# Optimization experiments

Measured on AMD Instinct MI355X. Metric: run time of the kernel, lower is better.

## Reference

```python
import jax, jax.numpy as jnp
import numpy as np

B, T, PHYS = 256, 64, 3        # batch of initial conditions, time steps, physical dim
LAT, NN, NHID = 8, 128, 3      # latent dim, hidden width, num hidden layers
WIN, PRED = 32, 64             # Hankel window, num_pred_steps


def _mlp(x, w_in, b_in, w_h, b_h, w_out, b_out):
    # Dense stack: relu hidden layers, linear output (ae_output_activation='linear')
    h = jax.nn.relu(x @ w_in + b_in)
    for i in range(w_h.shape[0]):
        h = jax.nn.relu(h @ w_h[i] + b_h[i])
    return h @ w_out + b_out


def _hankel_dmd(y):
    # y: [B, L, T] latent trajectories (already transposed as in call())
    Bsz, L, Tn = y.shape
    R = Tn - (WIN - 1)                                   # num_rows_hankel
    # Vectorized Hankel build (replaces nested TensorArray loops):
    idx = jnp.arange(R)[:, None] + jnp.arange(WIN)[None, :]
    H = y[:, :, idx].reshape(Bsz, L * R, WIN)
    Ym, Yp = H[:, :, :-1], H[:, :, 1:]
    # Exact DMD operator A = Yp V Sig^-1 U^H (full M x M, as in the TF code)
    U, sig, Vh = jnp.linalg.svd(Ym, full_matrices=False)
    V = jnp.swapaxes(Vh, -1, -2)
    A = Yp @ (V / sig[:, None, :]) @ jnp.swapaxes(U, -1, -2)     # [B, M, M]
    A = jax.lax.stop_gradient(A)   # no-op in fwd; eig has no JAX grad rule
    evals, evecs = jnp.linalg.eig(A)                             # complex64: [B,M], [B,M,M]
    Phi = jnp.linalg.solve(evecs, Ym.astype(evecs.dtype))
    y0 = Phi[:, :, 0]                                            # [B, M]
    evecs_s = evecs[:, ::R, :]                                   # stride = R -> [B, L, M]
    # Vectorized replacement of the sequential recon loop: evals^k for k=0..P-1
    powers = evals[:, None, :] ** jnp.arange(PRED)[None, :, None]  # [B, P, M]
    modes = powers * y0[:, None, :]                                # [B, P, M]
    recon = jnp.real(jnp.einsum('blm,bpm->bpl', evecs_s, modes))   # [B, P, L]
    return recon


def setup_inputs() -> dict:
    ks = jax.random.split(jax.random.key(0), 8)

    def w(k, fi, fo):
        return jax.random.normal(k, (fi, fo), jnp.float32) / np.sqrt(fi)

    def wh(k, f):
        return jax.random.normal(k, (NHID, f, f), jnp.float32) / np.sqrt(f)

    return {
        'x': jax.random.normal(ks[0], (B, T, PHYS), jnp.float32),
        'enc_w_in': w(ks[1], PHYS, NN), 'enc_b_in': jnp.zeros((NN,), jnp.float32),
        'enc_w_h': wh(ks[2], NN), 'enc_b_h': jnp.zeros((NHID, NN), jnp.float32),
        'enc_w_out': w(ks[3], NN, LAT), 'enc_b_out': jnp.zeros((LAT,), jnp.float32),
        'dec_w_in': w(ks[4], LAT, NN), 'dec_b_in': jnp.zeros((NN,), jnp.float32),
        'dec_w_h': wh(ks[5], NN), 'dec_b_h': jnp.zeros((NHID, NN), jnp.float32),
        'dec_w_out': w(ks[6], NN, PHYS), 'dec_b_out': jnp.zeros((PHYS,), jnp.float32),
    }


def reference(x, enc_w_in, enc_b_in, enc_w_h, enc_b_h, enc_w_out, enc_b_out,
              dec_w_in, dec_b_in, dec_w_h, dec_b_h, dec_w_out, dec_b_out):
    y = _mlp(x, enc_w_in, enc_b_in, enc_w_h, enc_b_h, enc_w_out, enc_b_out)        # [B, T, LAT]
    x_ae = _mlp(y, dec_w_in, dec_b_in, dec_w_h, dec_b_h, dec_w_out, dec_b_out)     # [B, T, PHYS]
    y_adv = _hankel_dmd(jnp.swapaxes(y, 1, 2))                                     # [B, PRED, LAT]
    x_adv = _mlp(y_adv, dec_w_in, dec_b_in, dec_w_h, dec_b_h, dec_w_out, dec_b_out)  # [B, PRED, PHYS]
    return (y, x_ae, x_adv, y_adv)
```

## Files before the change

kernel.cpp:

```cpp
#include <hip/hip_runtime.h>
#include <math.h>

namespace {
constexpr int kB = 256;
constexpr int kT = 64;
constexpr int kPhys = 3;
constexpr int kLat = 8;
constexpr int kNN = 128;
constexpr int kWin = 32;
constexpr int kPred = 64;
constexpr int kHRow = 132;
constexpr int kDecRows = 96;
constexpr int kThreads = 1024;
constexpr int kWUnit = 8 * 4 * 64 * 8;
}

typedef short bf16x8 __attribute__((ext_vector_type(8)));
typedef float f32x4 __attribute__((ext_vector_type(4)));

__device__ __forceinline__ double rdlane_f64(double x, int l) {
  const long long v = __double_as_longlong(x);
  const int lo = __builtin_amdgcn_readlane((int)(unsigned int)(v & 0xffffffffll), l);
  const int hi = __builtin_amdgcn_readlane((int)(v >> 32), l);
  const long long r = (((long long)hi) << 32) | (unsigned long long)(unsigned int)lo;
  return __longlong_as_double(r);
}

__device__ __forceinline__ unsigned rneb(float f) {
  const unsigned u = __float_as_uint(f);
  return (u + 0x7fffu + ((u >> 16) & 1u)) >> 16;
}
__device__ __forceinline__ void split3(float a, short& s1, short& s2, short& s3) {
  const unsigned b1 = rneb(a);
  const float f1 = __uint_as_float(b1 << 16);
  const float r1 = a - f1;
  const unsigned b2 = rneb(r1);
  const float f2 = __uint_as_float(b2 << 16);
  s1 = (short)b1; s2 = (short)b2; s3 = (short)rneb(r1 - f2);
}
__device__ __forceinline__ void split2(float a, short& s1, short& s2) {
  const unsigned b1 = rneb(a);
  const float f1 = __uint_as_float(b1 << 16);
  s1 = (short)b1; s2 = (short)rneb(a - f1);
}

__global__ __launch_bounds__(256) void split_weights_kernel(
    const float* __restrict__ ewh, const float* __restrict__ dwh,
    short* __restrict__ wfrag)
{
  const int gid = blockIdx.x * 256 + threadIdx.x;
  const int l = gid & 63;
  const int q = (gid >> 6) & 3;
  const int n = (gid >> 8) & 7;
  const int layer = gid >> 11;
  const bool enc = layer < 3;
  const float* __restrict__ W = enc ? (ewh + (size_t)layer * kNN * kNN)
                                    : (dwh + (size_t)(layer - 3) * kNN * kNN);
  const int colg = 16 * n + (l & 15);
  const int krow = 8 * (l >> 4);
  bf16x8 p1, p2, p3;
#pragma unroll
  for (int e = 0; e < 8; ++e) {
    const float wv = W[(32 * q + krow + e) * kNN + colg];
    short s1, s2, s3; split3(wv, s1, s2, s3);
    p1[e] = s1; p2[e] = s2; p3[e] = s3;
  }
  const int off = ((n * 4 + q) * 64 + l) * 8;
  if (enc) {
    const size_t base = (size_t)(layer * 3) * kWUnit;
    *(bf16x8*)&wfrag[base + off] = p1;
    *(bf16x8*)&wfrag[base + kWUnit + off] = p2;
    *(bf16x8*)&wfrag[base + 2 * kWUnit + off] = p3;
  } else {
    const size_t base = (size_t)(9 + (layer - 3) * 2) * kWUnit;
    *(bf16x8*)&wfrag[base + off] = p1;
    *(bf16x8*)&wfrag[base + kWUnit + off] = p2;
  }
}

template<int MT, int SPLITS>
__device__ __forceinline__ void pack_frag(const float* __restrict__ hb,
                                          short* __restrict__ frag, int tid)
{
  constexpr int PLANE = MT * 4 * 64 * 8;
  for (int idx = tid; idx < MT * 256; idx += kThreads) {
    const int m = idx >> 8, q = (idx >> 6) & 3, l = idx & 63;
    const int row = 16 * m + (l & 15), col = 32 * q + 8 * (l >> 4);
    const float4 f0 = *(const float4*)&hb[row * kHRow + col];
    const float4 f1 = *(const float4*)&hb[row * kHRow + col + 4];
    const float f[8] = {f0.x, f0.y, f0.z, f0.w, f1.x, f1.y, f1.z, f1.w};
    bf16x8 p1, p2, p3;
#pragma unroll
    for (int e = 0; e < 8; ++e) {
      if constexpr (SPLITS == 3) {
        short s1, s2, s3; split3(f[e], s1, s2, s3);
        p1[e] = s1; p2[e] = s2; p3[e] = s3;
      } else {
        short s1, s2; split2(f[e], s1, s2);
        p1[e] = s1; p2[e] = s2;
      }
    }
    const int o = ((m * 4 + q) * 64 + l) * 8;
    *(bf16x8*)&frag[o] = p1;
    *(bf16x8*)&frag[PLANE + o] = p2;
    if constexpr (SPLITS == 3) *(bf16x8*)&frag[2 * PLANE + o] = p3;
  }
}

template<int MPW, int SPLITS>
__device__ __forceinline__ void mfma_layer(
    const short* __restrict__ Bfrag, const float* __restrict__ bias,
    const short* __restrict__ frag, float* __restrict__ hb, int tid)
{
  constexpr int MT = 2 * MPW;
  constexpr int PLANE = MT * 4 * 64 * 8;
  const int w = tid >> 6, l = tid & 63;
  const int n = w & 7, m0 = (w >> 3) * MPW;
  const int colg = 16 * n + (l & 15);
  bf16x8 B1[4], B2[4], B3[4];
#pragma unroll
  for (int q = 0; q < 4; ++q) {
    const int boff = ((n * 4 + q) * 64 + l) * 8;
    B1[q] = *(const bf16x8*)&Bfrag[boff];
    B2[q] = *(const bf16x8*)&Bfrag[kWUnit + boff];
    if constexpr (SPLITS == 3) B3[q] = *(const bf16x8*)&Bfrag[2 * kWUnit + boff];
  }
  const float bj = bias[colg];
  f32x4 acc[MPW];
#pragma unroll
  for (int mi = 0; mi < MPW; ++mi) acc[mi] = {bj, bj, bj, bj};
#pragma unroll
  for (int q = 0; q < 4; ++q) {
#pragma unroll
    for (int mi = 0; mi < MPW; ++mi) {
      const int o = (((m0 + mi) * 4 + q) * 64 + l) * 8;
      const bf16x8 a1 = *(const bf16x8*)&frag[o];
      const bf16x8 a2 = *(const bf16x8*)&frag[PLANE + o];
      acc[mi] = __builtin_amdgcn_mfma_f32_16x16x32_bf16(a1, B1[q], acc[mi], 0, 0, 0);
      acc[mi] = __builtin_amdgcn_mfma_f32_16x16x32_bf16(a1, B2[q], acc[mi], 0, 0, 0);
      acc[mi] = __builtin_amdgcn_mfma_f32_16x16x32_bf16(a2, B1[q], acc[mi], 0, 0, 0);
      if constexpr (SPLITS == 3) {
        const bf16x8 a3 = *(const bf16x8*)&frag[2 * PLANE + o];
        acc[mi] = __builtin_amdgcn_mfma_f32_16x16x32_bf16(a1, B3[q], acc[mi], 0, 0, 0);
        acc[mi] = __builtin_amdgcn_mfma_f32_16x16x32_bf16(a2, B2[q], acc[mi], 0, 0, 0);
        acc[mi] = __builtin_amdgcn_mfma_f32_16x16x32_bf16(a3, B1[q], acc[mi], 0, 0, 0);
      }
    }
  }
  const int rbase = (l >> 4) * 4;
#pragma unroll
  for (int mi = 0; mi < MPW; ++mi)
#pragma unroll
    for (int r = 0; r < 4; ++r)
      hb[(16 * (m0 + mi) + rbase + r) * kHRow + colg] = fmaxf(acc[mi][r], 0.f);
}

__global__ __launch_bounds__(kThreads, 4) void fused_kernel(
    const float* __restrict__ x,
    const float* __restrict__ ewin, const float* __restrict__ ebin,
    const float* __restrict__ ebh,
    const float* __restrict__ ewout,const float* __restrict__ ebout,
    const float* __restrict__ dwin, const float* __restrict__ dbin,
    const float* __restrict__ dbh,
    const float* __restrict__ dwout,const float* __restrict__ dbout,
    const short* __restrict__ wfrag,
    float* __restrict__ y_g, float* __restrict__ xae_g,
    float* __restrict__ xadv_g, float* __restrict__ yadv_g)
{
  __shared__ float hb[kDecRows * kHRow];
  __shared__ __align__(16) char fragbuf[49152];
  __shared__ float ybuf[kT][kLat + 1];
  __shared__ float yadv2[kWin][kLat + 1];
  __shared__ float inb[kT][4];

  short* frag = (short*)fragbuf;
  double* dmd = (double*)fragbuf;
  double* yd   = dmd;
  double* P    = dmd + 520;
  double* Corr = dmd + 2664;
  double* KTm  = dmd + 3720;
  double* Dv   = dmd + 4743;

  const int tid = threadIdx.x;
  const int b = blockIdx.x;

  const float* __restrict__ xg = x + (size_t)b * kT * kPhys;
  for (int i = tid; i < kT * kPhys; i += kThreads) inb[i / 3][i % 3] = xg[i];
  __syncthreads();

  {
    const int j = tid & 127, rg = tid >> 7;
    const float w0 = ewin[j], w1 = ewin[kNN + j], w2 = ewin[2 * kNN + j];
    const float bj = ebin[j];
#pragma unroll
    for (int rr = 0; rr < 8; ++rr) {
      const int r = rg * 8 + rr;
      hb[r * kHRow + j] = fmaxf(bj + inb[r][0] * w0 + inb[r][1] * w1 + inb[r][2] * w2, 0.f);
    }
  }
  __syncthreads();

#pragma unroll
  for (int L = 0; L < 3; ++L) {
    pack_frag<4, 3>(hb, frag, tid);
    __syncthreads();
    mfma_layer<2, 3>(wfrag + (size_t)(L * 3) * kWUnit, ebh + L * kNN, frag, hb, tid);
    __syncthreads();
  }

  if (tid < 512) {
    const int r = tid >> 3, o = tid & 7;
    float a = ebout[o];
    for (int k4 = 0; k4 < kNN; k4 += 4) {
      const float4 hv = *(const float4*)&hb[r * kHRow + k4];
      a += hv.x * ewout[(k4 + 0) * kLat + o] + hv.y * ewout[(k4 + 1) * kLat + o]
         + hv.z * ewout[(k4 + 2) * kLat + o] + hv.w * ewout[(k4 + 3) * kLat + o];
    }
    ybuf[r][o] = a;
    y_g[(size_t)b * kT * kLat + tid] = a;
    yd[o * 65 + r] = (double)a;
  }
  __syncthreads();

  {
    for (int idx = tid; idx < 32 * 64; idx += kThreads) {
      const int d = idx >> 6, t = idx & 63;
      if (t + d < kT) {
        double s = 0.0;
#pragma unroll
        for (int l = 0; l < kLat; ++l) s += yd[l * 65 + t] * yd[l * 65 + t + d];
        P[d * 67 + t] = s;
      }
    }
    __syncthreads();

    {
      const int a = tid >> 5, c = tid & 31;
      const int d = (c >= a) ? (c - a) : (a - c);
      const int base = (c >= a) ? a : c;
      double s0 = 0.0, s1 = 0.0;
#pragma unroll
      for (int r = 0; r < 32; r += 2) { s0 += P[d * 67 + base + r]; s1 += P[d * 67 + base + r + 1]; }
      Corr[a * 33 + c] = s0 + s1 + P[d * 67 + base + 32];
    }
    __syncthreads();

    if (tid < 64) {
      const int lane = tid;
      const int colidx = (lane <= 30) ? lane : (lane <= 61 ? lane - 30 : 1);
      double m[31];
#pragma unroll
      for (int i = 0; i < 31; ++i) m[i] = Corr[i * 33 + colidx];
#pragma unroll
      for (int k = 0; k < 31; ++k) {
        const double piv = rdlane_f64(m[k], k);
        const double pinv = 1.0 / piv;
        m[k] *= pinv;
#pragma unroll
        for (int i = 0; i < 31; ++i) {
          if (i == k) continue;
          const double bci = rdlane_f64(m[i], k);
          m[i] = fma(-bci, m[k], m[i]);
        }
      }
      if (lane >= 31 && lane < 62) {
        const int c = lane - 31;
#pragma unroll
        for (int i = 0; i < 31; ++i) KTm[i * 33 + c] = m[i];
      }
      const int ri = (lane < 31) ? lane : 0;
      double Kr[31];
#pragma unroll
      for (int j = 0; j < 31; ++j) Kr[j] = KTm[ri * 33 + j];

      double dv = Kr[30];
      if (lane < 31) Dv[0 * 33 + lane] = dv;
      for (int k = 0; k < 31; ++k) {
        double a0 = 0.0, a1 = 0.0, a2 = 0.0, a3 = 0.0;
#pragma unroll
        for (int j = 0; j < 31; ++j) {
          const double dj = rdlane_f64(dv, j);
          if ((j & 3) == 0) a0 = fma(Kr[j], dj, a0);
          else if ((j & 3) == 1) a1 = fma(Kr[j], dj, a1);
          else if ((j & 3) == 2) a2 = fma(Kr[j], dj, a2);
          else a3 = fma(Kr[j], dj, a3);
        }
        dv = (a0 + a1) + (a2 + a3);
        if (lane < 31) Dv[(k + 1) * 33 + lane] = dv;
      }
    }
    __syncthreads();

    float* __restrict__ ob = yadv_g + (size_t)b * kPred * kLat;
    if (tid < 256) {
      ob[tid] = ybuf[tid >> 3][tid & 7];
    } else if (tid < 512) {
      const int q = tid - 256;
      const int k = q >> 3, l = q & 7;
      double a0 = 0.0, a1 = 0.0, a2 = 0.0, a3 = 0.0;
#pragma unroll
      for (int j = 0; j < 31; ++j) {
        const double t = yd[l * 65 + j + 1];
        if ((j & 3) == 0) a0 = fma(t, Dv[k * 33 + j], a0);
        else if ((j & 3) == 1) a1 = fma(t, Dv[k * 33 + j], a1);
        else if ((j & 3) == 2) a2 = fma(t, Dv[k * 33 + j], a2);
        else a3 = fma(t, Dv[k * 33 + j], a3);
      }
      const float v = (float)((a0 + a1) + (a2 + a3));
      ob[256 + q] = v;
      yadv2[k][l] = v;
    }
    __syncthreads();
  }

  {
    const int j = tid & 127, rg = tid >> 7;
    float wr[kLat];
#pragma unroll
    for (int k = 0; k < kLat; ++k) wr[k] = dwin[k * kNN + j];
    const float bj = dbin[j];
#pragma unroll
    for (int rr = 0; rr < 12; ++rr) {
      const int r = rg * 12 + rr;
      const float* __restrict__ src = (r < kT) ? &ybuf[r][0] : &yadv2[r - kT][0];
      float a = bj;
#pragma unroll
      for (int k = 0; k < kLat; ++k) a += src[k] * wr[k];
      hb[r * kHRow + j] = fmaxf(a, 0.f);
    }
  }
  __syncthreads();

#pragma unroll
  for (int L = 0; L < 3; ++L) {
    pack_frag<6, 2>(hb, frag, tid);
    __syncthreads();
    mfma_layer<3, 2>(wfrag + (size_t)(9 + L * 2) * kWUnit, dbh + L * kNN, frag, hb, tid);
    __syncthreads();
  }

  for (int idx = tid; idx < kDecRows * kPhys; idx += kThreads) {
    const int r = idx / 3, o = idx - r * 3;
    float a = dbout[o];
    for (int k4 = 0; k4 < kNN; k4 += 4) {
      const float4 hv = *(const float4*)&hb[r * kHRow + k4];
      a += hv.x * dwout[(k4 + 0) * kPhys + o] + hv.y * dwout[(k4 + 1) * kPhys + o]
         + hv.z * dwout[(k4 + 2) * kPhys + o] + hv.w * dwout[(k4 + 3) * kPhys + o];
    }
    if (r < kT) {
      xae_g[(size_t)b * kT * kPhys + idx] = a;
      if (r < kWin) xadv_g[(size_t)b * kT * kPhys + idx] = a;
    } else {
      const int rr = r - kT + kWin;
      xadv_g[(size_t)b * kT * kPhys + rr * kPhys + o] = a;
    }
  }
}

extern "C" void kernel_launch(void* const* d_in, const int* in_sizes, int n_in,
                              void* d_out, int out_size, void* d_ws, size_t ws_size,
                              hipStream_t stream)
{
  const float* x         = (const float*)d_in[0];
  const float* enc_w_in  = (const float*)d_in[1];
  const float* enc_b_in  = (const float*)d_in[2];
  const float* enc_w_h   = (const float*)d_in[3];
  const float* enc_b_h   = (const float*)d_in[4];
  const float* enc_w_out = (const float*)d_in[5];
  const float* enc_b_out = (const float*)d_in[6];
  const float* dec_w_in  = (const float*)d_in[7];
  const float* dec_b_in  = (const float*)d_in[8];
  const float* dec_w_h   = (const float*)d_in[9];
  const float* dec_b_h   = (const float*)d_in[10];
  const float* dec_w_out = (const float*)d_in[11];
  const float* dec_b_out = (const float*)d_in[12];

  float* out   = (float*)d_out;
  float* y     = out;
  float* x_ae  = out + (size_t)kB * kT * kLat;
  float* x_adv = x_ae + (size_t)kB * kT * kPhys;
  float* y_adv = x_adv + (size_t)kB * kT * kPhys;

  short* wfrag = (short*)d_ws;

  split_weights_kernel<<<48, 256, 0, stream>>>(enc_w_h, dec_w_h, wfrag);
  fused_kernel<<<kB, kThreads, 0, stream>>>(
      x, enc_w_in, enc_b_in, enc_b_h, enc_w_out, enc_b_out,
      dec_w_in, dec_b_in, dec_b_h, dec_w_out, dec_b_out,
      wfrag, y, x_ae, x_adv, y_adv);
}
```

Before: 57.19 us.

## Halve block to 512 threads and process MLP rows in two chunks

The block size drops from 1024 to 512 threads. The encoder and decoder MLP stacks now run on two row chunks (32 rows for the encoder, 48 for the decoder) instead of all rows at once. The hidden buffer and the fragment buffer share one union shared-memory region, which cuts LDS per block so more blocks can be resident per CU. The cost is roughly twice as many barriers and serial layer passes per block, and the weight fragments are reloaded for each chunk.

New measurement: 123.0 us. 115% more time.

```diff
diff --git a/kernel.cpp b/kernel.cpp
--- a/kernel.cpp
+++ b/kernel.cpp
@@ -10,8 +10,7 @@
 constexpr int kWin = 32;
 constexpr int kPred = 64;
 constexpr int kHRow = 132;
-constexpr int kDecRows = 96;
-constexpr int kThreads = 1024;
+constexpr int kThreads = 512;
 constexpr int kWUnit = 8 * 4 * 64 * 8;
 }
 
@@ -107,15 +106,13 @@
   }
 }
 
-template<int MPW, int SPLITS>
+template<int MT, int SPLITS>
 __device__ __forceinline__ void mfma_layer(
     const short* __restrict__ Bfrag, const float* __restrict__ bias,
     const short* __restrict__ frag, float* __restrict__ hb, int tid)
 {
-  constexpr int MT = 2 * MPW;
   constexpr int PLANE = MT * 4 * 64 * 8;
-  const int w = tid >> 6, l = tid & 63;
-  const int n = w & 7, m0 = (w >> 3) * MPW;
+  const int n = (tid >> 6) & 7, l = tid & 63;
   const int colg = 16 * n + (l & 15);
   bf16x8 B1[4], B2[4], B3[4];
 #pragma unroll
@@ -126,14 +123,14 @@
     if constexpr (SPLITS == 3) B3[q] = *(const bf16x8*)&Bfrag[2 * kWUnit + boff];
   }
   const float bj = bias[colg];
-  f32x4 acc[MPW];
-#pragma unroll
-  for (int mi = 0; mi < MPW; ++mi) acc[mi] = {bj, bj, bj, bj};
+  f32x4 acc[MT];
+#pragma unroll
+  for (int mi = 0; mi < MT; ++mi) acc[mi] = {bj, bj, bj, bj};
 #pragma unroll
   for (int q = 0; q < 4; ++q) {
 #pragma unroll
-    for (int mi = 0; mi < MPW; ++mi) {
-      const int o = (((m0 + mi) * 4 + q) * 64 + l) * 8;
+    for (int mi = 0; mi < MT; ++mi) {
+      const int o = ((mi * 4 + q) * 64 + l) * 8;
       const bf16x8 a1 = *(const bf16x8*)&frag[o];
       const bf16x8 a2 = *(const bf16x8*)&frag[PLANE + o];
       acc[mi] = __builtin_amdgcn_mfma_f32_16x16x32_bf16(a1, B1[q], acc[mi], 0, 0, 0);
@@ -149,10 +146,10 @@
   }
   const int rbase = (l >> 4) * 4;
 #pragma unroll
-  for (int mi = 0; mi < MPW; ++mi)
+  for (int mi = 0; mi < MT; ++mi)
 #pragma unroll
     for (int r = 0; r < 4; ++r)
-      hb[(16 * (m0 + mi) + rbase + r) * kHRow + colg] = fmaxf(acc[mi][r], 0.f);
+      hb[(16 * mi + rbase + r) * kHRow + colg] = fmaxf(acc[mi][r], 0.f);
 }
 
 __global__ __launch_bounds__(kThreads, 4) void fused_kernel(
@@ -167,58 +164,68 @@
     float* __restrict__ y_g, float* __restrict__ xae_g,
     float* __restrict__ xadv_g, float* __restrict__ yadv_g)
 {
-  __shared__ float hb[kDecRows * kHRow];
-  __shared__ __align__(16) char fragbuf[49152];
-  __shared__ float ybuf[kT][kLat + 1];
-  __shared__ float yadv2[kWin][kLat + 1];
+  __shared__ __align__(16) char US[49920];
+  __shared__ float ybuf[kT * kLat];
+  __shared__ float yadv2[kWin * kLat];
   __shared__ float inb[kT][4];
 
-  short* frag = (short*)fragbuf;
-  double* dmd = (double*)fragbuf;
+  const int tid = threadIdx.x;
+  const int b = blockIdx.x;
+
+  double* dmd  = (double*)US;
   double* yd   = dmd;
   double* P    = dmd + 520;
   double* Corr = dmd + 2664;
   double* KTm  = dmd + 3720;
   double* Dv   = dmd + 4743;
 
-  const int tid = threadIdx.x;
-  const int b = blockIdx.x;
-
   const float* __restrict__ xg = x + (size_t)b * kT * kPhys;
   for (int i = tid; i < kT * kPhys; i += kThreads) inb[i / 3][i % 3] = xg[i];
   __syncthreads();
 
   {
-    const int j = tid & 127, rg = tid >> 7;
-    const float w0 = ewin[j], w1 = ewin[kNN + j], w2 = ewin[2 * kNN + j];
-    const float bj = ebin[j];
-#pragma unroll
-    for (int rr = 0; rr < 8; ++rr) {
-      const int r = rg * 8 + rr;
-      hb[r * kHRow + j] = fmaxf(bj + inb[r][0] * w0 + inb[r][1] * w1 + inb[r][2] * w2, 0.f);
-    }
-  }
-  __syncthreads();
-
-#pragma unroll
-  for (int L = 0; L < 3; ++L) {
-    pack_frag<4, 3>(hb, frag, tid);
-    __syncthreads();
-    mfma_layer<2, 3>(wfrag + (size_t)(L * 3) * kWUnit, ebh + L * kNN, frag, hb, tid);
-    __syncthreads();
-  }
-
-  if (tid < 512) {
+    float* hb = (float*)US;
+    short* frag = (short*)(US + 16896);
+    for (int ch = 0; ch < 2; ++ch) {
+      const int r0 = ch * 32;
+      {
+        const int j = tid & 127, rg = tid >> 7;
+        const float w0 = ewin[j], w1 = ewin[kNN + j], w2 = ewin[2 * kNN + j];
+        const float bj = ebin[j];
+#pragma unroll
+        for (int rr = 0; rr < 8; ++rr) {
+          const int r = rg * 8 + rr;
+          const int gr = r0 + r;
+          hb[r * kHRow + j] =
+              fmaxf(bj + inb[gr][0] * w0 + inb[gr][1] * w1 + inb[gr][2] * w2, 0.f);
+        }
+      }
+      __syncthreads();
+#pragma unroll
+      for (int L = 0; L < 3; ++L) {
+        pack_frag<2, 3>(hb, frag, tid);
+        __syncthreads();
+        mfma_layer<2, 3>(wfrag + (size_t)(L * 3) * kWUnit, ebh + L * kNN, frag, hb, tid);
+        __syncthreads();
+      }
+      if (tid < 256) {
+        const int r = tid >> 3, o = tid & 7;
+        float a = ebout[o];
+        for (int k4 = 0; k4 < kNN; k4 += 4) {
+          const float4 hv = *(const float4*)&hb[r * kHRow + k4];
+          a += hv.x * ewout[(k4 + 0) * kLat + o] + hv.y * ewout[(k4 + 1) * kLat + o]
+             + hv.z * ewout[(k4 + 2) * kLat + o] + hv.w * ewout[(k4 + 3) * kLat + o];
+        }
+        ybuf[(r0 + r) * kLat + o] = a;
+        y_g[(size_t)b * kT * kLat + (r0 + r) * kLat + o] = a;
+      }
+      __syncthreads();
+    }
+  }
+
+  {
     const int r = tid >> 3, o = tid & 7;
-    float a = ebout[o];
-    for (int k4 = 0; k4 < kNN; k4 += 4) {
-      const float4 hv = *(const float4*)&hb[r * kHRow + k4];
-      a += hv.x * ewout[(k4 + 0) * kLat + o] + hv.y * ewout[(k4 + 1) * kLat + o]
-         + hv.z * ewout[(k4 + 2) * kLat + o] + hv.w * ewout[(k4 + 3) * kLat + o];
-    }
-    ybuf[r][o] = a;
-    y_g[(size_t)b * kT * kLat + tid] = a;
-    yd[o * 65 + r] = (double)a;
+    yd[o * 65 + r] = (double)ybuf[r * kLat + o];
   }
   __syncthreads();
 
@@ -234,8 +241,8 @@
     }
     __syncthreads();
 
-    {
-      const int a = tid >> 5, c = tid & 31;
+    for (int idx = tid; idx < 32 * 32; idx += kThreads) {
+      const int a = idx >> 5, c = idx & 31;
       const int d = (c >= a) ? (c - a) : (a - c);
       const int base = (c >= a) ? a : c;
       double s0 = 0.0, s1 = 0.0;
@@ -293,8 +300,8 @@
 
     float* __restrict__ ob = yadv_g + (size_t)b * kPred * kLat;
     if (tid < 256) {
-      ob[tid] = ybuf[tid >> 3][tid & 7];
-    } else if (tid < 512) {
+      ob[tid] = ybuf[tid];
+    } else {
       const int q = tid - 256;
       const int k = q >> 3, l = q & 7;
       double a0 = 0.0, a1 = 0.0, a2 = 0.0, a3 = 0.0;
@@ -308,51 +315,60 @@
       }
       const float v = (float)((a0 + a1) + (a2 + a3));
       ob[256 + q] = v;
-      yadv2[k][l] = v;
+      yadv2[q] = v;
     }
     __syncthreads();
   }
 
   {
-    const int j = tid & 127, rg = tid >> 7;
-    float wr[kLat];
-#pragma unroll
-    for (int k = 0; k < kLat; ++k) wr[k] = dwin[k * kNN + j];
-    const float bj = dbin[j];
-#pragma unroll
-    for (int rr = 0; rr < 12; ++rr) {
-      const int r = rg * 12 + rr;
-      const float* __restrict__ src = (r < kT) ? &ybuf[r][0] : &yadv2[r - kT][0];
-      float a = bj;
-#pragma unroll
-      for (int k = 0; k < kLat; ++k) a += src[k] * wr[k];
-      hb[r * kHRow + j] = fmaxf(a, 0.f);
-    }
-  }
-  __syncthreads();
-
-#pragma unroll
-  for (int L = 0; L < 3; ++L) {
-    pack_frag<6, 2>(hb, frag, tid);
-    __syncthreads();
-    mfma_layer<3, 2>(wfrag + (size_t)(9 + L * 2) * kWUnit, dbh + L * kNN, frag, hb, tid);
-    __syncthreads();
-  }
-
-  for (int idx = tid; idx < kDecRows * kPhys; idx += kThreads) {
-    const int r = idx / 3, o = idx - r * 3;
-    float a = dbout[o];
-    for (int k4 = 0; k4 < kNN; k4 += 4) {
-      const float4 hv = *(const float4*)&hb[r * kHRow + k4];
-      a += hv.x * dwout[(k4 + 0) * kPhys + o] + hv.y * dwout[(k4 + 1) * kPhys + o]
-         + hv.z * dwout[(k4 + 2) * kPhys + o] + hv.w * dwout[(k4 + 3) * kPhys + o];
-    }
-    if (r < kT) {
-      xae_g[(size_t)b * kT * kPhys + idx] = a;
-      if (r < kWin) xadv_g[(size_t)b * kT * kPhys + idx] = a;
-    } else {
-      const int rr = r - kT + kWin;
-      xadv_g[(size_t)b * kT * kPhys + rr * kPhys + o] = a;
+    float* hb = (float*)US;
+    short* frag = (short*)(US + 25344);
+    for (int ch = 0; ch < 2; ++ch) {
+      const int R0 = ch * 48;
+      {
+        const int j = tid & 127, rg = tid >> 7;
+        float wr[kLat];
+#pragma unroll
+        for (int k = 0; k < kLat; ++k) wr[k] = dwin[k * kNN + j];
+        const float bj = dbin[j];
+#pragma unroll
+        for (int rr = 0; rr < 12; ++rr) {
+          const int r = rg * 12 + rr;
+          const int gr = R0 + r;
+          const float* __restrict__ src =
+              (gr < kT) ? &ybuf[gr * kLat] : &yadv2[(gr - kT) * kLat];
+          float a = bj;
+#pragma unroll
+          for (int k = 0; k < kLat; ++k) a += src[k] * wr[k];
+          hb[r * kHRow + j] = fmaxf(a, 0.f);
+        }
+      }
+      __syncthreads();
+#pragma unroll
+      for (int L = 0; L < 3; ++L) {
+        pack_frag<3, 2>(hb, frag, tid);
+        __syncthreads();
+        mfma_layer<3, 2>(wfrag + (size_t)(9 + L * 2) * kWUnit, dbh + L * kNN, frag, hb, tid);
+        __syncthreads();
+      }
+      if (tid < 144) {
+        const int r = tid / 3, o = tid - r * 3;
+        const int gr = R0 + r;
+        float a = dbout[o];
+        for (int k4 = 0; k4 < kNN; k4 += 4) {
+          const float4 hv = *(const float4*)&hb[r * kHRow + k4];
+          a += hv.x * dwout[(k4 + 0) * kPhys + o] + hv.y * dwout[(k4 + 1) * kPhys + o]
+             + hv.z * dwout[(k4 + 2) * kPhys + o] + hv.w * dwout[(k4 + 3) * kPhys + o];
+        }
+        if (gr < kT) {
+          xae_g[(size_t)b * kT * kPhys + gr * kPhys + o] = a;
+          if (gr < kWin) xadv_g[(size_t)b * kT * kPhys + gr * kPhys + o] = a;
+        } else {
+          const int rr = gr - kT + kWin;
+          xadv_g[(size_t)b * kT * kPhys + rr * kPhys + o] = a;
+        }
+      }
+      __syncthreads();
     }
   }
 }
```
